# Kernel tuning notes

Measured on AMD Instinct MI355X. Metric: run time of the kernel, lower is better.

The kernel has to match this reference:

```python
import jax, jax.numpy as jnp
import numpy as np

N, C1, C2, H, W, NH = 4, 512, 512, 32, 32, 8


def _conv(x, w, pad):
    return jax.lax.conv_general_dilated(
        x, w, window_strides=(1, 1), padding=[(pad, pad), (pad, pad)],
        dimension_numbers=("NCHW", "OIHW", "NCHW"))


def _heads(t, n, c, nh):
    # [n, c, h, w] -> [n, nh, c, hw//nh] (spatial dim split across heads)
    return jnp.transpose(t.reshape(n, c, nh, -1), (0, 2, 1, 3))


def _attend(q, k, v):
    # q:[n,nh,Sq,d] k,v:[n,nh,Sk,d]; fp32 math as in the original
    scale = 1.0 / np.sqrt(k.shape[-1])
    att = jnp.einsum("nhqd,nhkd->nhqk", q.astype(jnp.float32), k.astype(jnp.float32)) * scale
    att = jax.nn.softmax(att, axis=-1)
    return jnp.einsum("nhqk,nhkd->nhqd", att, v.astype(jnp.float32))


def setup_inputs() -> dict:
    key = jax.random.key(0)
    ks = jax.random.split(key, 11)
    s = 0.02
    inp = {
        "x_l": jax.random.normal(ks[0], (N, C1, H, W), jnp.float32),
        "x_g": jax.random.normal(ks[1], (N, C2, H, W), jnp.float32),
        "Wk1": jax.random.normal(ks[2], (C1, C1, 3, 3), jnp.float32) * s,
        "Wq1": jax.random.normal(ks[3], (C1, C1, 3, 3), jnp.float32) * s,
        "Wv1": jax.random.normal(ks[4], (C1, C1, 3, 3), jnp.float32) * s,
        "Wk2": jax.random.normal(ks[5], (C2, C2, 3, 3), jnp.float32) * s,
        "Wq2": jax.random.normal(ks[6], (C2, C2, 3, 3), jnp.float32) * s,
        "Wv2": jax.random.normal(ks[7], (C2, C2, 3, 3), jnp.float32) * s,
        "Wp1": jax.random.normal(ks[8], (C1, C1, 1, 1), jnp.float32) * s,
        "Wp2": jax.random.normal(ks[9], (C2, C2, 1, 1), jnp.float32) * s,
        "resweight": jnp.ones((), jnp.float32),  # init 0 in torch; 1 used so the branch is active
    }
    return inp


def reference(x_l, x_g, Wk1, Wq1, Wv1, Wk2, Wq2, Wv2, Wp1, Wp2, resweight):
    n, c1, h, w = x_l.shape
    c2 = x_g.shape[1]
    k_l = _heads(_conv(x_l, Wk1, 1), n, c1, NH)
    q_l = _heads(_conv(x_l, Wq1, 1), n, c1, NH)
    v_l = _heads(_conv(x_l, Wv1, 1), n, c1, NH)
    k_g = _heads(_conv(x_g, Wk2, 1), n, c2, NH)
    q_g = _heads(_conv(x_g, Wq2, 1), n, c2, NH)
    v_g = _heads(_conv(x_g, Wv2, 1), n, c2, NH)

    # global queries attend over local keys/values
    y_g = _attend(q_g, k_l, v_l)                       # [n, nh, c2, hw/nh]
    y_g = jnp.transpose(y_g, (0, 2, 1, 3)).reshape(n, c2, h, w)
    y_g = _conv(y_g, Wp2, 0)

    # local queries attend over global keys/values
    y_l = _attend(q_l, k_g, v_g)                       # [n, nh, c1, hw/nh]
    y_l = jnp.transpose(y_l, (0, 2, 1, 3)).reshape(n, c1, h, w)
    y_l = _conv(y_l, Wp1, 0)

    return (x_l + y_l * resweight, x_g + y_g * resweight)
```

## Files before the change

### kernel.cpp

```cpp
#include <hip/hip_runtime.h>
#include <hip/hip_bf16.h>
#include <stdint.h>

typedef unsigned short u16;
typedef unsigned int u32;

#define TSLOT 2097152
#define IC_ELEMS 37748736ull
#define WB_ELEMS 14155776ull
#define WPB_ELEMS 524288ull

typedef __attribute__((ext_vector_type(8))) short short8;
typedef __attribute__((ext_vector_type(8))) unsigned short u16x8;
typedef __attribute__((ext_vector_type(4))) float f32x4;

__device__ __forceinline__ float bf2f(u16 u) {
    union { u32 i; float f; } v; v.i = ((u32)u) << 16; return v.f;
}
__device__ __forceinline__ u16 f2bf(float f) {
    union { u32 i; float f; } v; v.f = f;
    u32 u = v.i;
    return (u16)((u + 0x7FFFu + ((u >> 16) & 1u)) >> 16);
}
__device__ __forceinline__ u32 pkbf(float a, float b) {
    __hip_bfloat162 h = __float22bfloat162_rn(make_float2(a, b));
    u32 u; __builtin_memcpy(&u, &h, 4); return u;
}

__device__ __forceinline__ void gl_lds16(const u16* g, u16* l) {
    __builtin_amdgcn_global_load_lds(
        (const __attribute__((address_space(1))) void*)(uintptr_t)(const void*)g,
        (__attribute__((address_space(3))) void*)(uintptr_t)(void*)l,
        16, 0, 0);
}

__global__ __launch_bounds__(256) void prep_all(
    const float* __restrict__ xl, const float* __restrict__ xg,
    const float* __restrict__ w0, const float* __restrict__ w1,
    const float* __restrict__ w2, const float* __restrict__ w3,
    const float* __restrict__ w4, const float* __restrict__ w5,
    const float* __restrict__ wp1, const float* __restrict__ wp2,
    u16* __restrict__ wbf, u16* __restrict__ ic, u16* __restrict__ wpb)
{
    __shared__ float xs[32][4][32];
    const int b = blockIdx.x;
    const int t = threadIdx.x;

    if (b < 3456) {
        const int tsr = b / 576, inner = b - tsr * 576;
        const float* src = tsr == 0 ? w0 : tsr == 1 ? w1 : tsr == 2 ? w2
                         : tsr == 3 ? w3 : tsr == 4 ? w4 : w5;
        const size_t base = (size_t)inner * 4096 + t * 16;
        u16* dst = wbf + (size_t)tsr * 2359296 + base;
        const float4* s4 = (const float4*)(src + base);
        float4 f0 = s4[0], f1 = s4[1], f2 = s4[2], f3 = s4[3];
        u32 p[4];
        p[0] = pkbf(f0.x, f0.y); p[1] = pkbf(f0.z, f0.w);
        p[2] = pkbf(f1.x, f1.y); p[3] = pkbf(f1.z, f1.w);
        *(uint4*)dst = *(uint4*)p;
        p[0] = pkbf(f2.x, f2.y); p[1] = pkbf(f2.z, f2.w);
        p[2] = pkbf(f3.x, f3.y); p[3] = pkbf(f3.z, f3.w);
        *(uint4*)(dst + 8) = *(uint4*)p;
        return;
    }
    if (b >= 5504) {
        const int b3 = b - 5504;
        const float* src = (b3 < 64) ? wp1 : wp2;
        const size_t base = (size_t)(b3 & 63) * 4096 + t * 16;
        u16* dst = wpb + ((b3 < 64) ? 0 : 262144) + base;
        const float4* s4 = (const float4*)(src + base);
        float4 f0 = s4[0], f1 = s4[1], f2 = s4[2], f3 = s4[3];
        u32 p[4];
        p[0] = pkbf(f0.x, f0.y); p[1] = pkbf(f0.z, f0.w);
        p[2] = pkbf(f1.x, f1.y); p[3] = pkbf(f1.z, f1.w);
        *(uint4*)dst = *(uint4*)p;
        p[0] = pkbf(f2.x, f2.y); p[1] = pkbf(f2.z, f2.w);
        p[2] = pkbf(f3.x, f3.y); p[3] = pkbf(f3.z, f3.w);
        *(uint4*)(dst + 8) = *(uint4*)p;
        return;
    }

    const int b2 = b - 3456;
    const int mt = b2 >> 4;
    const int ct = b2 & 15;
    const int m0 = mt * 64;
    const int img  = m0 >> 12;
    const int m_in = m0 & 4095;
    const int n_i  = m_in >> 10;
    const int y0   = (m_in & 1023) >> 5;

    const float* xp = (img ? xg : xl) + ((size_t)n_i * 512 + ct * 32) * 1024;

    for (int v = t; v < 4096; v += 256) {
        int ci = v >> 7;
        int r  = (v >> 5) & 3;
        int xx = v & 31;
        int yy = y0 - 1 + r;
        xs[ci][r][xx] = ((unsigned)yy < 32u) ? xp[ci * 1024 + yy * 32 + xx] : 0.f;
    }
    __syncthreads();

    const int m_local = t >> 2;
    const int q       = t & 3;
    const int y_sel   = m_local >> 5;
    const int x       = m_local & 31;
    u16* orow = ic + (size_t)(m0 + m_local) * 4608 + (size_t)(ct * 32 + q * 8) * 9;

    #pragma unroll
    for (int c = 0; c < 9; ++c) {
        u16x8 st;
        #pragma unroll
        for (int u = 0; u < 8; ++u) {
            const int e   = c * 8 + u;
            const int cil = q * 8 + e / 9;
            const int tap = e % 9;
            const int ky  = tap / 3, kx = tap % 3;
            int xx = x + kx - 1;
            float v = ((unsigned)xx < 32u) ? xs[cil][y_sel + ky][xx] : 0.f;
            st[u] = f2bf(v);
        }
        *(u16x8*)(orow + c * 8) = st;
    }
}

__global__ __launch_bounds__(256) void conv_gemm(
    const u16* __restrict__ ic, const u16* __restrict__ wbf,
    u16* __restrict__ kl, u16* __restrict__ ql, u16* __restrict__ vl,
    u16* __restrict__ kg, u16* __restrict__ qg, u16* __restrict__ vg)
{
    __shared__ __align__(16) u16 A_lds[128 * 64];
    __shared__ __align__(16) u16 B_lds[128 * 64];

    const int t  = threadIdx.x;
    const int mt = blockIdx.x;
    const int nt = blockIdx.y;
    const int img = mt >> 5;
    const int wt  = nt >> 2;
    const int co0 = (nt & 3) * 128;
    const int m0  = mt * 128;

    u16* osel = img == 0 ? (wt == 0 ? kl : wt == 1 ? ql : vl)
                         : (wt == 0 ? kg : wt == 1 ? qg : vg);
    const u16* wsel = wbf + (size_t)(img * 3 + wt) * 2359296;

    const int lane = t & 63;
    const int w4   = t >> 6;

    const int s_rb  = w4 * 8 + (lane >> 3);
    const int s_col = ((lane & 7) ^ (lane >> 3)) * 8;
    const u16* agp[4];
    const u16* bgp[4];
    #pragma unroll
    for (int i = 0; i < 4; ++i) {
        agp[i] = ic   + (size_t)(m0  + s_rb + i * 32) * 4608 + s_col;
        bgp[i] = wsel + (size_t)(co0 + s_rb + i * 32) * 4608 + s_col;
    }
    u16* Adst = A_lds + w4 * 512;
    u16* Bdst = B_lds + w4 * 512;

    const int wm = (w4 & 1) * 64;
    const int wn = (w4 >> 1) * 64;
    const int fr = lane & 15;
    const int qd = lane >> 4;
    int arow[4], brow[4];
    #pragma unroll
    for (int i = 0; i < 4; ++i) {
        arow[i] = wm + i * 16 + fr;
        brow[i] = wn + i * 16 + fr;
    }

    f32x4 acc[4][4] = {};

    for (int kb = 0; kb < 4608; kb += 64) {
        __syncthreads();
        #pragma unroll
        for (int i = 0; i < 4; ++i) {
            gl_lds16(agp[i] + kb, Adst + i * 2048);
            gl_lds16(bgp[i] + kb, Bdst + i * 2048);
        }
        __syncthreads();
        #pragma unroll
        for (int ks = 0; ks < 2; ++ks) {
            short8 af[4], bq[4];
            #pragma unroll
            for (int i = 0; i < 4; ++i) {
                int c = (ks * 4 + qd) ^ (arow[i] & 7);
                af[i] = *(const short8*)&A_lds[arow[i] * 64 + c * 8];
            }
            #pragma unroll
            for (int j = 0; j < 4; ++j) {
                int c = (ks * 4 + qd) ^ (brow[j] & 7);
                bq[j] = *(const short8*)&B_lds[brow[j] * 64 + c * 8];
            }
            #pragma unroll
            for (int i = 0; i < 4; ++i)
                #pragma unroll
                for (int j = 0; j < 4; ++j)
                    acc[i][j] = __builtin_amdgcn_mfma_f32_16x16x32_bf16(
                        af[i], bq[j], acc[i][j], 0, 0, 0);
        }
    }

    const int m_in = m0 & 4095;
    const int n_i  = m_in >> 10;
    const int head = (m_in & 1023) >> 7;
    u16* ob = osel + (size_t)(n_i * 8 + head) * 65536;
    if (wt == 2) {
        #pragma unroll
        for (int i = 0; i < 4; ++i) {
            int dd0 = wm + i * 16 + qd * 4;
            #pragma unroll
            for (int j = 0; j < 4; ++j) {
                int co = co0 + wn + j * 16 + fr;
                #pragma unroll
                for (int r = 0; r < 4; ++r)
                    ob[(size_t)(dd0 + r) * 512 + co] = f2bf(acc[i][j][r]);
            }
        }
    } else {
        #pragma unroll
        for (int i = 0; i < 4; ++i) {
            int dd0 = wm + i * 16 + qd * 4;
            #pragma unroll
            for (int j = 0; j < 4; ++j) {
                int co = co0 + wn + j * 16 + fr;
                ushort4 st;
                st.x = f2bf(acc[i][j][0]); st.y = f2bf(acc[i][j][1]);
                st.z = f2bf(acc[i][j][2]); st.w = f2bf(acc[i][j][3]);
                *(ushort4*)(ob + (size_t)co * 128 + dd0) = st;
            }
        }
    }
}

__global__ __launch_bounds__(256) void attn_mfma(
    const u16* __restrict__ Q0, const u16* __restrict__ K0,
    const u16* __restrict__ V0, u16* __restrict__ O0,
    const u16* __restrict__ Q1, const u16* __restrict__ K1,
    const u16* __restrict__ V1, u16* __restrict__ O1)
{
    __shared__ __align__(16) u16 Qlo[64 * 64];
    __shared__ __align__(16) u16 Qhi[64 * 64];
    __shared__ __align__(16) u16 Klo[64 * 64];
    __shared__ __align__(16) u16 Khi[64 * 64];
    __shared__ __align__(16) u16 Vs[128 * 64];
    __shared__ u16 Ps[64][72];

    const int t    = threadIdx.x;
    const int lane = t & 63;
    const int w    = t >> 6;
    const int qt   = blockIdx.x;
    const int nh   = blockIdx.y;
    const int z    = blockIdx.z;

    const u16* Q = (z ? Q1 : Q0) + (size_t)nh * 65536;
    const u16* K = (z ? K1 : K0) + (size_t)nh * 65536;
    const u16* V = (z ? V1 : V0) + (size_t)nh * 65536;
    u16*       O = (z ? O1 : O0) + (size_t)nh * 65536;

    const int q0    = qt * 64;
    const int s_rb  = w * 8 + (lane >> 3);
    const int s_col = ((lane & 7) ^ (lane >> 3)) * 8;
    u16* const dQl = Qlo + w * 512;
    u16* const dQh = Qhi + w * 512;
    u16* const dKl = Klo + w * 512;
    u16* const dKh = Khi + w * 512;
    u16* const dV  = Vs  + w * 512;

    #pragma unroll
    for (int i = 0; i < 2; ++i) {
        const u16* qr = Q + (size_t)(q0 + s_rb + i * 32) * 128;
        gl_lds16(qr + s_col,      dQl + i * 2048);
        gl_lds16(qr + 64 + s_col, dQh + i * 2048);
    }

    const int fr  = lane & 15;
    const int qd  = lane >> 4;
    const int koq = qd * 8;

    float m_run[4] = {-3e38f, -3e38f, -3e38f, -3e38f};
    float l_run[4] = {0.f, 0.f, 0.f, 0.f};
    f32x4 Ot[8] = {};
    const float scale = 0.08838834764831845f;

    for (int cb = 0; cb < 8; ++cb) {
        __syncthreads();
        const int kb = cb * 64;
        #pragma unroll
        for (int i = 0; i < 2; ++i) {
            const u16* kr = K + (size_t)(kb + s_rb + i * 32) * 128;
            gl_lds16(kr + s_col,      dKl + i * 2048);
            gl_lds16(kr + 64 + s_col, dKh + i * 2048);
        }
        #pragma unroll
        for (int i = 0; i < 4; ++i)
            gl_lds16(V + (size_t)(s_rb + i * 32) * 512 + kb + s_col, dV + i * 2048);
        __syncthreads();

        f32x4 s[4] = {};
        #pragma unroll
        for (int dstep = 0; dstep < 4; ++dstep) {
            const u16* Qh = (dstep < 2) ? Qlo : Qhi;
            const u16* Kh = (dstep < 2) ? Klo : Khi;
            const int cq = (((dstep & 1) * 4 + qd) ^ (fr & 7)) * 8;
            short8 a = *(const short8*)&Qh[(w * 16 + fr) * 64 + cq];
            #pragma unroll
            for (int nj = 0; nj < 4; ++nj) {
                short8 b = *(const short8*)&Kh[(nj * 16 + fr) * 64 + cq];
                s[nj] = __builtin_amdgcn_mfma_f32_16x16x32_bf16(a, b, s[nj], 0, 0, 0);
            }
        }

        float al[4];
        #pragma unroll
        for (int r = 0; r < 4; ++r) {
            float mc = fmaxf(fmaxf(s[0][r], s[1][r]), fmaxf(s[2][r], s[3][r])) * scale;
            mc = fmaxf(mc, __shfl_xor(mc, 1));
            mc = fmaxf(mc, __shfl_xor(mc, 2));
            mc = fmaxf(mc, __shfl_xor(mc, 4));
            mc = fmaxf(mc, __shfl_xor(mc, 8));
            float mn = fmaxf(m_run[r], mc);
            al[r] = __expf(m_run[r] - mn);
            m_run[r] = mn;
            float rs = 0.f;
            #pragma unroll
            for (int nj = 0; nj < 4; ++nj) {
                float p = __expf(s[nj][r] * scale - mn);
                s[nj][r] = p;
                rs += p;
            }
            rs += __shfl_xor(rs, 1);
            rs += __shfl_xor(rs, 2);
            rs += __shfl_xor(rs, 4);
            rs += __shfl_xor(rs, 8);
            l_run[r] = l_run[r] * al[r] + rs;
        }

        #pragma unroll
        for (int nj = 0; nj < 4; ++nj)
            #pragma unroll
            for (int r = 0; r < 4; ++r)
                Ps[w * 16 + qd * 4 + r][nj * 16 + fr] = f2bf(s[nj][r]);

        {
            int srcl = (fr >> 2) << 4;
            float a0 = __shfl(al[0], srcl), a1 = __shfl(al[1], srcl);
            float a2 = __shfl(al[2], srcl), a3 = __shfl(al[3], srcl);
            int rsel = fr & 3;
            float ac = rsel == 0 ? a0 : rsel == 1 ? a1 : rsel == 2 ? a2 : a3;
            #pragma unroll
            for (int t8 = 0; t8 < 8; ++t8)
                #pragma unroll
                for (int r = 0; r < 4; ++r)
                    Ot[t8][r] *= ac;
        }

        #pragma unroll
        for (int ks = 0; ks < 2; ++ks) {
            short8 b = *(const short8*)&Ps[w * 16 + fr][ks * 32 + koq];
            #pragma unroll
            for (int t8 = 0; t8 < 8; ++t8) {
                const int cv = ((ks * 4 + qd) ^ (fr & 7)) * 8;
                short8 a = *(const short8*)&Vs[(t8 * 16 + fr) * 64 + cv];
                Ot[t8] = __builtin_amdgcn_mfma_f32_16x16x32_bf16(a, b, Ot[t8], 0, 0, 0);
            }
        }
    }

    int srcl = (fr >> 2) << 4;
    float l0 = __shfl(l_run[0], srcl), l1 = __shfl(l_run[1], srcl);
    float l2 = __shfl(l_run[2], srcl), l3 = __shfl(l_run[3], srcl);
    int rsel = fr & 3;
    float lc = rsel == 0 ? l0 : rsel == 1 ? l1 : rsel == 2 ? l2 : l3;
    float linv = 1.0f / lc;
    int c = q0 + w * 16 + fr;
    #pragma unroll
    for (int t8 = 0; t8 < 8; ++t8)
        #pragma unroll
        for (int r = 0; r < 4; ++r) {
            int d = t8 * 16 + qd * 4 + r;
            O[(size_t)d * 512 + c] = f2bf(Ot[t8][r] * linv);
        }
}

__global__ __launch_bounds__(256) void proj_mfma(
    const u16* __restrict__ wpb,
    const u16* __restrict__ Otl, const u16* __restrict__ Otg,
    const float* __restrict__ x_l, const float* __restrict__ x_g,
    const float* __restrict__ rwp,
    float* __restrict__ out0, float* __restrict__ out1)
{
    __shared__ __align__(16) u16 A_lds[128 * 64];
    __shared__ __align__(16) u16 B_lds[128 * 64];

    const int t  = threadIdx.x;
    const int ct = blockIdx.x;
    const int st = blockIdx.y;
    const int z  = blockIdx.z;
    const int which = z >> 2;
    const int nn    = z & 3;

    const u16*   Wp = wpb + (which ? 262144 : 0);
    const u16*   Ot = (which ? Otg : Otl) + (size_t)nn * 524288;
    const float* xr = (which ? x_g : x_l) + (size_t)nn * 524288;
    float*     outp = (which ? out1 : out0) + (size_t)nn * 524288;

    const int co0 = ct * 128, s0 = st * 128;
    const int lane = t & 63;
    const int w4   = t >> 6;

    const int s_rb  = w4 * 8 + (lane >> 3);
    const int s_col = ((lane & 7) ^ (lane >> 3)) * 8;
    const u16* agp[4];
    const u16* bgp[4];
    #pragma unroll
    for (int i = 0; i < 4; ++i) {
        agp[i] = Wp + (size_t)(co0 + s_rb + i * 32) * 512 + s_col;
        bgp[i] = Ot + (size_t)(s0  + s_rb + i * 32) * 512 + s_col;
    }
    u16* Adst = A_lds + w4 * 512;
    u16* Bdst = B_lds + w4 * 512;

    const int wm = (w4 & 1) * 64;
    const int wn = (w4 >> 1) * 64;
    const int fr = lane & 15;
    const int qd = lane >> 4;
    int arow[4], brow[4];
    #pragma unroll
    for (int i = 0; i < 4; ++i) {
        arow[i] = wm + i * 16 + fr;
        brow[i] = wn + i * 16 + fr;
    }

    f32x4 acc[4][4] = {};

    for (int kb = 0; kb < 512; kb += 64) {
        __syncthreads();
        #pragma unroll
        for (int i = 0; i < 4; ++i) {
            gl_lds16(agp[i] + kb, Adst + i * 2048);
            gl_lds16(bgp[i] + kb, Bdst + i * 2048);
        }
        __syncthreads();
        #pragma unroll
        for (int ks = 0; ks < 2; ++ks) {
            short8 af[4], bq[4];
            #pragma unroll
            for (int i = 0; i < 4; ++i) {
                int c = (ks * 4 + qd) ^ (arow[i] & 7);
                af[i] = *(const short8*)&A_lds[arow[i] * 64 + c * 8];
            }
            #pragma unroll
            for (int j = 0; j < 4; ++j) {
                int c = (ks * 4 + qd) ^ (brow[j] & 7);
                bq[j] = *(const short8*)&B_lds[brow[j] * 64 + c * 8];
            }
            #pragma unroll
            for (int i = 0; i < 4; ++i)
                #pragma unroll
                for (int j = 0; j < 4; ++j)
                    acc[i][j] = __builtin_amdgcn_mfma_f32_16x16x32_bf16(
                        af[i], bq[j], acc[i][j], 0, 0, 0);
        }
    }

    const float rwv = *rwp;
    #pragma unroll
    for (int i = 0; i < 4; ++i) {
        int co_b = co0 + wm + i * 16 + qd * 4;
        #pragma unroll
        for (int j = 0; j < 4; ++j) {
            int s = s0 + wn + j * 16 + fr;
            #pragma unroll
            for (int r = 0; r < 4; ++r) {
                size_t a = (size_t)(co_b + r) * 1024 + s;
                outp[a] = xr[a] + rwv * acc[i][j][r];
            }
        }
    }
}

extern "C" void kernel_launch(void* const* d_in, const int* in_sizes, int n_in,
                              void* d_out, int out_size, void* d_ws, size_t ws_size,
                              hipStream_t stream) {
    const float* x_l = (const float*)d_in[0];
    const float* x_g = (const float*)d_in[1];
    const float* Wk1 = (const float*)d_in[2];
    const float* Wq1 = (const float*)d_in[3];
    const float* Wv1 = (const float*)d_in[4];
    const float* Wk2 = (const float*)d_in[5];
    const float* Wq2 = (const float*)d_in[6];
    const float* Wv2 = (const float*)d_in[7];
    const float* Wp1 = (const float*)d_in[8];
    const float* Wp2 = (const float*)d_in[9];
    const float* rw  = (const float*)d_in[10];

    u16* ws  = (u16*)d_ws;
    u16* ic  = ws;
    u16* wbf = ws + IC_ELEMS;
    u16* Kl  = wbf + WB_ELEMS;
    u16* Ql  = Kl  + TSLOT;
    u16* Vtl = Ql  + TSLOT;
    u16* Kg  = Vtl + TSLOT;
    u16* Qg  = Kg  + TSLOT;
    u16* Vtg = Qg  + TSLOT;
    u16* Otg = Vtg + TSLOT;
    u16* Otl = Otg + TSLOT;
    u16* wpb = Otl + TSLOT;

    float* out0 = (float*)d_out;
    float* out1 = out0 + (size_t)TSLOT;

    prep_all<<<5632, 256, 0, stream>>>(
        x_l, x_g, Wk1, Wq1, Wv1, Wk2, Wq2, Wv2, Wp1, Wp2, wbf, ic, wpb);

    conv_gemm<<<dim3(64, 12), 256, 0, stream>>>(
        ic, wbf, Kl, Ql, Vtl, Kg, Qg, Vtg);

    attn_mfma<<<dim3(8, 32, 2), 256, 0, stream>>>(
        Qg, Kl, Vtl, Otg, Ql, Kg, Vtg, Otl);

    proj_mfma<<<dim3(4, 8, 8), 256, 0, stream>>>(
        wpb, Otl, Otg, x_l, x_g, rw, out0, out1);
}
```

Measured before the change: 348.8 us.

## Replace explicit im2col with implicit-GEMM conv over padded NHWC input

The prep kernel stops writing a full im2col matrix (about 38M bf16 elements). It now writes a zero-padded NHWC bf16 copy of the inputs and reorders the conv weights to tap-major, channel-minor order. The conv GEMM builds its A-tile addresses directly from the padded tensor using a per-k-block tap offset, which removes a large global write and re-read. The attention kernel also loads its Q fragments into registers once, reusing the K LDS buffers, which frees the dedicated Q shared memory. The weight transpose through LDS adds a strided scalar gather in prep, and A-tile loads now come from overlapping windows rather than contiguous rows.

```diff
diff --git a/kernel.cpp b/kernel.cpp
--- a/kernel.cpp
+++ b/kernel.cpp
@@ -6,7 +6,7 @@
 typedef unsigned int u32;
 
 #define TSLOT 2097152
-#define IC_ELEMS 37748736ull
+#define XT_ELEMS 4734976ull
 #define WB_ELEMS 14155776ull
 #define WPB_ELEMS 524288ull
 
@@ -14,9 +14,6 @@
 typedef __attribute__((ext_vector_type(8))) unsigned short u16x8;
 typedef __attribute__((ext_vector_type(4))) float f32x4;
 
-__device__ __forceinline__ float bf2f(u16 u) {
-    union { u32 i; float f; } v; v.i = ((u32)u) << 16; return v.f;
-}
 __device__ __forceinline__ u16 f2bf(float f) {
     union { u32 i; float f; } v; v.f = f;
     u32 u = v.i;
@@ -40,91 +37,79 @@
     const float* __restrict__ w2, const float* __restrict__ w3,
     const float* __restrict__ w4, const float* __restrict__ w5,
     const float* __restrict__ wp1, const float* __restrict__ wp2,
-    u16* __restrict__ wbf, u16* __restrict__ ic, u16* __restrict__ wpb)
+    u16* __restrict__ xt, u16* __restrict__ wbf, u16* __restrict__ wpb)
 {
-    __shared__ float xs[32][4][32];
+    __shared__ u16 sh[4608];
     const int b = blockIdx.x;
     const int t = threadIdx.x;
 
-    if (b < 3456) {
-        const int tsr = b / 576, inner = b - tsr * 576;
-        const float* src = tsr == 0 ? w0 : tsr == 1 ? w1 : tsr == 2 ? w2
-                         : tsr == 3 ? w3 : tsr == 4 ? w4 : w5;
-        const size_t base = (size_t)inner * 4096 + t * 16;
-        u16* dst = wbf + (size_t)tsr * 2359296 + base;
-        const float4* s4 = (const float4*)(src + base);
-        float4 f0 = s4[0], f1 = s4[1], f2 = s4[2], f3 = s4[3];
-        u32 p[4];
-        p[0] = pkbf(f0.x, f0.y); p[1] = pkbf(f0.z, f0.w);
-        p[2] = pkbf(f1.x, f1.y); p[3] = pkbf(f1.z, f1.w);
-        *(uint4*)dst = *(uint4*)p;
-        p[0] = pkbf(f2.x, f2.y); p[1] = pkbf(f2.z, f2.w);
-        p[2] = pkbf(f3.x, f3.y); p[3] = pkbf(f3.z, f3.w);
-        *(uint4*)(dst + 8) = *(uint4*)p;
+    if (b < 1088) {
+        const int nimg = b / 136;
+        const int rem  = b - nimg * 136;
+        const int yy   = rem >> 2;
+        const int cig  = rem & 3;
+        const int img  = nimg >> 2, n = nimg & 3;
+        const float* srcx = (img ? xg : xl);
+        u16* ob = xt + (((size_t)nimg * 34 + yy) * 34) * 512 + cig * 128;
+
+        u16 (*xls)[132] = (u16(*)[132])sh;
+        const bool interior = (yy >= 1 && yy <= 32);
+        if (interior) {
+            for (int v = t; v < 4096; v += 256) {
+                int ci_l = v >> 5, xx0 = v & 31;
+                float vv = srcx[(((size_t)n * 512 + cig * 128 + ci_l) * 32 + (yy - 1)) * 32 + xx0];
+                xls[xx0][ci_l] = f2bf(vv);
+            }
+            __syncthreads();
+        }
+        for (int v = t; v < 544; v += 256) {
+            int xx = v >> 4, l16 = v & 15;
+            u16x8 st;
+            if (interior && xx >= 1 && xx <= 32) {
+                #pragma unroll
+                for (int j = 0; j < 8; ++j) st[j] = xls[xx - 1][l16 * 8 + j];
+            } else {
+                #pragma unroll
+                for (int j = 0; j < 8; ++j) st[j] = 0;
+            }
+            *(u16x8*)(ob + (size_t)xx * 512 + l16 * 8) = st;
+        }
         return;
     }
-    if (b >= 5504) {
-        const int b3 = b - 5504;
-        const float* src = (b3 < 64) ? wp1 : wp2;
-        const size_t base = (size_t)(b3 & 63) * 4096 + t * 16;
-        u16* dst = wpb + ((b3 < 64) ? 0 : 262144) + base;
-        const float4* s4 = (const float4*)(src + base);
-        float4 f0 = s4[0], f1 = s4[1], f2 = s4[2], f3 = s4[3];
-        u32 p[4];
-        p[0] = pkbf(f0.x, f0.y); p[1] = pkbf(f0.z, f0.w);
-        p[2] = pkbf(f1.x, f1.y); p[3] = pkbf(f1.z, f1.w);
-        *(uint4*)dst = *(uint4*)p;
-        p[0] = pkbf(f2.x, f2.y); p[1] = pkbf(f2.z, f2.w);
-        p[2] = pkbf(f3.x, f3.y); p[3] = pkbf(f3.z, f3.w);
-        *(uint4*)(dst + 8) = *(uint4*)p;
+    if (b < 4160) {
+        const int idx = b - 1088;
+        const int wt = idx >> 9, co = idx & 511;
+        const float* srcw = wt == 0 ? w0 : wt == 1 ? w1 : wt == 2 ? w2
+                          : wt == 3 ? w3 : wt == 4 ? w4 : w5;
+        const float* wr = srcw + (size_t)co * 4608;
+        #pragma unroll
+        for (int j = 0; j < 18; ++j)
+            sh[t * 18 + j] = f2bf(wr[t * 18 + j]);
+        __syncthreads();
+        u16* orow = wbf + ((size_t)wt * 512 + co) * 4608;
+        for (int v = t; v < 4608; v += 256) {
+            int tap = v >> 9, ci = v & 511;
+            orow[v] = sh[ci * 9 + tap];
+        }
         return;
     }
-
-    const int b2 = b - 3456;
-    const int mt = b2 >> 4;
-    const int ct = b2 & 15;
-    const int m0 = mt * 64;
-    const int img  = m0 >> 12;
-    const int m_in = m0 & 4095;
-    const int n_i  = m_in >> 10;
-    const int y0   = (m_in & 1023) >> 5;
-
-    const float* xp = (img ? xg : xl) + ((size_t)n_i * 512 + ct * 32) * 1024;
-
-    for (int v = t; v < 4096; v += 256) {
-        int ci = v >> 7;
-        int r  = (v >> 5) & 3;
-        int xx = v & 31;
-        int yy = y0 - 1 + r;
-        xs[ci][r][xx] = ((unsigned)yy < 32u) ? xp[ci * 1024 + yy * 32 + xx] : 0.f;
-    }
-    __syncthreads();
-
-    const int m_local = t >> 2;
-    const int q       = t & 3;
-    const int y_sel   = m_local >> 5;
-    const int x       = m_local & 31;
-    u16* orow = ic + (size_t)(m0 + m_local) * 4608 + (size_t)(ct * 32 + q * 8) * 9;
-
-    #pragma unroll
-    for (int c = 0; c < 9; ++c) {
-        u16x8 st;
-        #pragma unroll
-        for (int u = 0; u < 8; ++u) {
-            const int e   = c * 8 + u;
-            const int cil = q * 8 + e / 9;
-            const int tap = e % 9;
-            const int ky  = tap / 3, kx = tap % 3;
-            int xx = x + kx - 1;
-            float v = ((unsigned)xx < 32u) ? xs[cil][y_sel + ky][xx] : 0.f;
-            st[u] = f2bf(v);
-        }
-        *(u16x8*)(orow + c * 8) = st;
-    }
+    const int b3 = b - 4160;
+    const float* src = (b3 < 64) ? wp1 : wp2;
+    const size_t base = (size_t)(b3 & 63) * 4096 + t * 16;
+    u16* dst = wpb + ((b3 < 64) ? 0 : 262144) + base;
+    const float4* s4 = (const float4*)(src + base);
+    float4 f0 = s4[0], f1 = s4[1], f2 = s4[2], f3 = s4[3];
+    u32 p[4];
+    p[0] = pkbf(f0.x, f0.y); p[1] = pkbf(f0.z, f0.w);
+    p[2] = pkbf(f1.x, f1.y); p[3] = pkbf(f1.z, f1.w);
+    *(uint4*)dst = *(uint4*)p;
+    p[0] = pkbf(f2.x, f2.y); p[1] = pkbf(f2.z, f2.w);
+    p[2] = pkbf(f3.x, f3.y); p[3] = pkbf(f3.z, f3.w);
+    *(uint4*)(dst + 8) = *(uint4*)p;
 }
 
 __global__ __launch_bounds__(256) void conv_gemm(
-    const u16* __restrict__ ic, const u16* __restrict__ wbf,
+    const u16* __restrict__ xt, const u16* __restrict__ wbf,
     u16* __restrict__ kl, u16* __restrict__ ql, u16* __restrict__ vl,
     u16* __restrict__ kg, u16* __restrict__ qg, u16* __restrict__ vg)
 {
@@ -138,10 +123,11 @@
     const int wt  = nt >> 2;
     const int co0 = (nt & 3) * 128;
     const int m0  = mt * 128;
+    const int nimg = m0 >> 10;
+    const int y0   = (m0 & 1023) >> 5;
 
     u16* osel = img == 0 ? (wt == 0 ? kl : wt == 1 ? ql : vl)
                          : (wt == 0 ? kg : wt == 1 ? qg : vg);
-    const u16* wsel = wbf + (size_t)(img * 3 + wt) * 2359296;
 
     const int lane = t & 63;
     const int w4   = t >> 6;
@@ -152,8 +138,11 @@
     const u16* bgp[4];
     #pragma unroll
     for (int i = 0; i < 4; ++i) {
-        agp[i] = ic   + (size_t)(m0  + s_rb + i * 32) * 4608 + s_col;
-        bgp[i] = wsel + (size_t)(co0 + s_rb + i * 32) * 4608 + s_col;
+        int ri = s_rb + i * 32;
+        int yy = y0 + (ri >> 5);
+        int xx = ri & 31;
+        agp[i] = xt + (((size_t)nimg * 34 + yy) * 34 + xx) * 512 + s_col;
+        bgp[i] = wbf + ((size_t)(img * 3 + wt) * 512 + co0 + s_rb + i * 32) * 4608 + s_col;
     }
     u16* Adst = A_lds + w4 * 512;
     u16* Bdst = B_lds + w4 * 512;
@@ -172,11 +161,15 @@
     f32x4 acc[4][4] = {};
 
     for (int kb = 0; kb < 4608; kb += 64) {
+        const int tap = kb >> 9;
+        const int ci0 = kb & 511;
+        const int ky = tap / 3, kx = tap - ky * 3;
+        const int toff = (ky * 34 + kx) * 512 + ci0;
         __syncthreads();
         #pragma unroll
         for (int i = 0; i < 4; ++i) {
-            gl_lds16(agp[i] + kb, Adst + i * 2048);
-            gl_lds16(bgp[i] + kb, Bdst + i * 2048);
+            gl_lds16(agp[i] + toff, Adst + i * 2048);
+            gl_lds16(bgp[i] + kb,   Bdst + i * 2048);
         }
         __syncthreads();
         #pragma unroll
@@ -239,8 +232,6 @@
     const u16* __restrict__ Q1, const u16* __restrict__ K1,
     const u16* __restrict__ V1, u16* __restrict__ O1)
 {
-    __shared__ __align__(16) u16 Qlo[64 * 64];
-    __shared__ __align__(16) u16 Qhi[64 * 64];
     __shared__ __align__(16) u16 Klo[64 * 64];
     __shared__ __align__(16) u16 Khi[64 * 64];
     __shared__ __align__(16) u16 Vs[128 * 64];
@@ -261,22 +252,28 @@
     const int q0    = qt * 64;
     const int s_rb  = w * 8 + (lane >> 3);
     const int s_col = ((lane & 7) ^ (lane >> 3)) * 8;
-    u16* const dQl = Qlo + w * 512;
-    u16* const dQh = Qhi + w * 512;
     u16* const dKl = Klo + w * 512;
     u16* const dKh = Khi + w * 512;
     u16* const dV  = Vs  + w * 512;
 
-    #pragma unroll
-    for (int i = 0; i < 2; ++i) {
-        const u16* qr = Q + (size_t)(q0 + s_rb + i * 32) * 128;
-        gl_lds16(qr + s_col,      dQl + i * 2048);
-        gl_lds16(qr + 64 + s_col, dQh + i * 2048);
-    }
-
     const int fr  = lane & 15;
     const int qd  = lane >> 4;
     const int koq = qd * 8;
+
+    #pragma unroll
+    for (int i = 0; i < 2; ++i) {
+        const u16* qr = Q + (size_t)(q0 + s_rb + i * 32) * 128;
+        gl_lds16(qr + s_col,      dKl + i * 2048);
+        gl_lds16(qr + 64 + s_col, dKh + i * 2048);
+    }
+    __syncthreads();
+    short8 aq[4];
+    #pragma unroll
+    for (int dstep = 0; dstep < 4; ++dstep) {
+        const u16* Qh = (dstep < 2) ? Klo : Khi;
+        const int cq = (((dstep & 1) * 4 + qd) ^ (fr & 7)) * 8;
+        aq[dstep] = *(const short8*)&Qh[(w * 16 + fr) * 64 + cq];
+    }
 
     float m_run[4] = {-3e38f, -3e38f, -3e38f, -3e38f};
     float l_run[4] = {0.f, 0.f, 0.f, 0.f};
@@ -300,14 +297,12 @@
         f32x4 s[4] = {};
         #pragma unroll
         for (int dstep = 0; dstep < 4; ++dstep) {
-            const u16* Qh = (dstep < 2) ? Qlo : Qhi;
             const u16* Kh = (dstep < 2) ? Klo : Khi;
             const int cq = (((dstep & 1) * 4 + qd) ^ (fr & 7)) * 8;
-            short8 a = *(const short8*)&Qh[(w * 16 + fr) * 64 + cq];
             #pragma unroll
             for (int nj = 0; nj < 4; ++nj) {
-                short8 b = *(const short8*)&Kh[(nj * 16 + fr) * 64 + cq];
-                s[nj] = __builtin_amdgcn_mfma_f32_16x16x32_bf16(a, b, s[nj], 0, 0, 0);
+                short8 bkf = *(const short8*)&Kh[(nj * 16 + fr) * 64 + cq];
+                s[nj] = __builtin_amdgcn_mfma_f32_16x16x32_bf16(aq[dstep], bkf, s[nj], 0, 0, 0);
             }
         }
 
@@ -496,8 +491,8 @@
     const float* rw  = (const float*)d_in[10];
 
     u16* ws  = (u16*)d_ws;
-    u16* ic  = ws;
-    u16* wbf = ws + IC_ELEMS;
+    u16* xt  = ws;
+    u16* wbf = ws + XT_ELEMS;
     u16* Kl  = wbf + WB_ELEMS;
     u16* Ql  = Kl  + TSLOT;
     u16* Vtl = Ql  + TSLOT;
@@ -511,11 +506,11 @@
     float* out0 = (float*)d_out;
     float* out1 = out0 + (size_t)TSLOT;
 
-    prep_all<<<5632, 256, 0, stream>>>(
-        x_l, x_g, Wk1, Wq1, Wv1, Wk2, Wq2, Wv2, Wp1, Wp2, wbf, ic, wpb);
+    prep_all<<<4288, 256, 0, stream>>>(
+        x_l, x_g, Wk1, Wq1, Wv1, Wk2, Wq2, Wv2, Wp1, Wp2, xt, wbf, wpb);
 
     conv_gemm<<<dim3(64, 12), 256, 0, stream>>>(
-        ic, wbf, Kl, Ql, Vtl, Kg, Qg, Vtg);
+        xt, wbf, Kl, Ql, Vtl, Kg, Qg, Vtg);
 
     attn_mfma<<<dim3(8, 32, 2), 256, 0, stream>>>(
         Qg, Kl, Vtl, Otg, Ql, Kg, Vtg, Otl);
```

After: 339.7 us. 1.03x faster.
